# Optimization experiments

Hardware: AMD Instinct MI355X
Metric: run time of the kernel (lower is better)

Reference implementation:

```python
import jax, jax.numpy as jnp
import numpy as np

N, E, B, D = 50000, 1600000, 256, 64


def _lin(k, fan_in, fan_out):
    kw, kb = jax.random.split(k)
    bound = 1.0 / np.sqrt(fan_in)
    w = jax.random.uniform(kw, (fan_in, fan_out), jnp.float32, -bound, bound)
    b = jax.random.uniform(kb, (fan_out,), jnp.float32, -bound, bound)
    return w, b


def setup_inputs() -> dict:
    key = jax.random.key(0)
    ks = jax.random.split(key, 16)
    inp = {
        "x": jax.random.normal(ks[0], (N, D), jnp.float32),
        "edge_attr": jax.random.normal(ks[1], (E, D), jnp.float32),
        "u": jax.random.normal(ks[2], (B, D), jnp.float32),
        "edge_index": jax.random.randint(ks[3], (2, E), 0, N, jnp.int32),
        "batch": jnp.sort(jax.random.randint(ks[4], (N,), 0, B, jnp.int32)),
    }
    # three MLPs: edge (in 4D), node (in 3D), global (in 3D); dims [2D, 2D, D]
    specs = [("e", 4 * D), ("n", 3 * D), ("g", 3 * D)]
    ki = 5
    for name, in_dim in specs:
        dims = [in_dim, 2 * D, 2 * D, D]
        for li in range(3):
            w, b = _lin(ks[ki], dims[li], dims[li + 1]); ki += 1
            inp[f"{name}w{li+1}"] = w
            inp[f"{name}b{li+1}"] = b
    return inp


def _mlp(h, w1, b1, w2, b2, w3, b3):
    h = h @ w1 + b1
    h = jax.nn.relu(h) @ w2 + b2
    h = jax.nn.relu(h) @ w3 + b3
    return h


def _scatter_mean(src, idx, num_segments):
    s = jax.ops.segment_sum(src, idx, num_segments=num_segments)
    c = jax.ops.segment_sum(jnp.ones_like(src[:, :1]), idx, num_segments=num_segments)
    return s / jnp.maximum(c, 1.0)


def reference(x, edge_attr, u,
              ew1, eb1, ew2, eb2, ew3, eb3,
              nw1, nb1, nw2, nb2, nw3, nb3,
              gw1, gb1, gw2, gb2, gw3, gb3,
              edge_index, batch):
    row, col = edge_index[0], edge_index[1]
    # edge model: cat[src, dest, edge_attr, u[batch[row]]] -> MLP
    e_in = jnp.concatenate([x[row], x[col], edge_attr, u[batch[row]]], axis=1)  # [E, 4D]
    e = _mlp(e_in, ew1, eb1, ew2, eb2, ew3, eb3)  # [E, D]
    # node model: scatter_mean(edge_attr', row) cat x cat u[batch] -> MLP
    n_agg = _scatter_mean(e, row, x.shape[0])  # [N, D]
    n_in = jnp.concatenate([n_agg, x, u[batch]], axis=1)  # [N, 3D]
    xn = _mlp(n_in, nw1, nb1, nw2, nb2, nw3, nb3)  # [N, D]
    # global model: cat[u, scatter_mean(x', batch), scatter_mean(e', batch[row])]
    edge_mean = _scatter_mean(e, batch[row], u.shape[0])  # [B, D]
    node_mean = _scatter_mean(xn, batch, u.shape[0])  # [B, D]
    g_in = jnp.concatenate([u, node_mean, edge_mean], axis=1)  # [B, 3D]
    un = _mlp(g_in, gw1, gb1, gw2, gb2, gw3, gb3)  # [B, D]
    return xn, e, un
```

## Files before the change

kernel.cpp:

```cpp
#include <hip/hip_runtime.h>

#define NN 50000
#define EE 1600000
#define BBATCH 256
#define DD 64

typedef _Float16 f16;
typedef _Float16 f16x4 __attribute__((ext_vector_type(4)));
typedef _Float16 f16x8 __attribute__((ext_vector_type(8)));
typedef float f32x4 __attribute__((ext_vector_type(4)));

#define MFMA16(a,b,c) __builtin_amdgcn_mfma_f32_16x16x32_f16((a),(b),(c),0,0,0)

constexpr int EW1_RL  = 264;
constexpr int EW1_OFF = 0;
constexpr int EW2_OFF = EW1_OFF + 128 * EW1_RL;
constexpr int EW3_OFF = EW2_OFF + 128 * 136;
constexpr int EH_OFF  = EW3_OFF + 64 * 136;
constexpr int EB_OFF  = EH_OFF + 8 * 16 * 136;
constexpr int ELDS    = EB_OFF + 640;

constexpr int NW1_RL  = 200;
constexpr int NW1_OFF = 0;
constexpr int NW2_OFF = NW1_OFF + 128 * NW1_RL;
constexpr int NW3_OFF = NW2_OFF + 128 * 136;
constexpr int NH_OFF  = NW3_OFF + 64 * 136;
constexpr int NB_OFF  = NH_OFF + 4 * 32 * 136;
constexpr int NLDS    = NB_OFF + 640;

__device__ __forceinline__ f16x8 pack8(const float* __restrict__ p) {
  f32x4 a = *(const f32x4*)p;
  f32x4 b = *(const f32x4*)(p + 4);
  f16x8 r;
  r[0]=(f16)a[0]; r[1]=(f16)a[1]; r[2]=(f16)a[2]; r[3]=(f16)a[3];
  r[4]=(f16)b[0]; r[5]=(f16)b[1]; r[6]=(f16)b[2]; r[7]=(f16)b[3];
  return r;
}
__device__ __forceinline__ f16x8 pack8s(const float* __restrict__ p, float sc) {
  f32x4 a = *(const f32x4*)p;
  f32x4 b = *(const f32x4*)(p + 4);
  a = a * sc; b = b * sc;
  f16x8 r;
  r[0]=(f16)a[0]; r[1]=(f16)a[1]; r[2]=(f16)a[2]; r[3]=(f16)a[3];
  r[4]=(f16)b[0]; r[5]=(f16)b[1]; r[6]=(f16)b[2]; r[7]=(f16)b[3];
  return r;
}
__device__ __forceinline__ f16x8 cvt8(f32x4 a, f32x4 b) {
  f16x8 r;
  r[0]=(f16)a[0]; r[1]=(f16)a[1]; r[2]=(f16)a[2]; r[3]=(f16)a[3];
  r[4]=(f16)b[0]; r[5]=(f16)b[1]; r[6]=(f16)b[2]; r[7]=(f16)b[3];
  return r;
}

template<int KSL, int W1RL, int W1O, int W2O, int W3O>
__device__ __forceinline__ void mlp3_core(f16* __restrict__ sm,
    const float* __restrict__ b1l, const float* __restrict__ b2l,
    const float* __restrict__ b3l,
    const f16x8 (&A1)[2][KSL], const int hb, const int r15, const int g,
    f32x4 (&acc3)[2][4])
{
  #pragma unroll
  for (int hh = 0; hh < 2; ++hh) {
    f32x4 acc[2][4];
    #pragma unroll
    for (int nt = 0; nt < 4; ++nt) {
      const float bv = b1l[(hh*4 + nt)*16 + r15];
      acc[0][nt] = (f32x4){bv, bv, bv, bv};
      acc[1][nt] = acc[0][nt];
    }
    #pragma unroll
    for (int s = 0; s < KSL; ++s) {
      #pragma unroll
      for (int nt = 0; nt < 4; ++nt) {
        const f16x8 bf = *(const f16x8*)&sm[W1O + ((hh*4+nt)*16 + r15) * W1RL + s*32 + g*8];
        acc[0][nt] = MFMA16(A1[0][s], bf, acc[0][nt]);
        acc[1][nt] = MFMA16(A1[1][s], bf, acc[1][nt]);
      }
    }
    #pragma unroll
    for (int mt = 0; mt < 2; ++mt)
      #pragma unroll
      for (int nt = 0; nt < 4; ++nt)
        #pragma unroll
        for (int i = 0; i < 4; ++i)
          sm[hb + (mt*16 + g*4 + i)*136 + (hh*4+nt)*16 + r15] =
              (f16)fmaxf(acc[mt][nt][i], 0.f);
  }

  f16x8 A2[2][4];
  #pragma unroll
  for (int mt = 0; mt < 2; ++mt)
    #pragma unroll
    for (int s = 0; s < 4; ++s)
      A2[mt][s] = *(const f16x8*)&sm[hb + (mt*16 + r15)*136 + s*32 + g*8];

  #pragma unroll
  for (int hh = 0; hh < 2; ++hh) {
    f32x4 acc[2][4];
    #pragma unroll
    for (int nt = 0; nt < 4; ++nt) {
      const float bv = b2l[(hh*4 + nt)*16 + r15];
      acc[0][nt] = (f32x4){bv, bv, bv, bv};
      acc[1][nt] = acc[0][nt];
    }
    #pragma unroll
    for (int s = 0; s < 4; ++s) {
      #pragma unroll
      for (int nt = 0; nt < 4; ++nt) {
        const f16x8 bf = *(const f16x8*)&sm[W2O + ((hh*4+nt)*16 + r15)*136 + s*32 + g*8];
        acc[0][nt] = MFMA16(A2[0][s], bf, acc[0][nt]);
        acc[1][nt] = MFMA16(A2[1][s], bf, acc[1][nt]);
      }
    }
    #pragma unroll
    for (int mt = 0; mt < 2; ++mt)
      #pragma unroll
      for (int nt = 0; nt < 4; ++nt)
        #pragma unroll
        for (int i = 0; i < 4; ++i)
          sm[hb + (mt*16 + g*4 + i)*136 + (hh*4+nt)*16 + r15] =
              (f16)fmaxf(acc[mt][nt][i], 0.f);
  }

  f16x8 A3[2][4];
  #pragma unroll
  for (int mt = 0; mt < 2; ++mt)
    #pragma unroll
    for (int s = 0; s < 4; ++s)
      A3[mt][s] = *(const f16x8*)&sm[hb + (mt*16 + r15)*136 + s*32 + g*8];

  #pragma unroll
  for (int nt = 0; nt < 4; ++nt) {
    const float bv = b3l[nt*16 + r15];
    acc3[0][nt] = (f32x4){bv, bv, bv, bv};
    acc3[1][nt] = acc3[0][nt];
  }
  #pragma unroll
  for (int s = 0; s < 4; ++s) {
    #pragma unroll
    for (int nt = 0; nt < 4; ++nt) {
      const f16x8 bf = *(const f16x8*)&sm[W3O + (nt*16 + r15)*136 + s*32 + g*8];
      acc3[0][nt] = MFMA16(A3[0][s], bf, acc3[0][nt]);
      acc3[1][nt] = MFMA16(A3[1][s], bf, acc3[1][nt]);
    }
  }
}

__global__ void transpose_all(
    const float* __restrict__ e1, const float* __restrict__ e2, const float* __restrict__ e3,
    const float* __restrict__ n1, const float* __restrict__ n2, const float* __restrict__ n3,
    const float* __restrict__ q1, const float* __restrict__ q2, const float* __restrict__ q3,
    f16* __restrict__ dst) {
  int tid = blockIdx.x * 256 + threadIdx.x;
  const int o1=32768,o2=49152,o3=57344,o4=81920,o5=98304,o6=106496,o7=131072,o8=147456,o9=155648;
  if (tid >= o9) return;
  const float* src; int in, od, rel;
  if      (tid < o1) { src=e1; in=256; od=128; rel=tid;    }
  else if (tid < o2) { src=e2; in=128; od=128; rel=tid-o1; }
  else if (tid < o3) { src=e3; in=128; od=64;  rel=tid-o2; }
  else if (tid < o4) { src=n1; in=192; od=128; rel=tid-o3; }
  else if (tid < o5) { src=n2; in=128; od=128; rel=tid-o4; }
  else if (tid < o6) { src=n3; in=128; od=64;  rel=tid-o5; }
  else if (tid < o7) { src=q1; in=192; od=128; rel=tid-o6; }
  else if (tid < o8) { src=q2; in=128; od=128; rel=tid-o7; }
  else               { src=q3; in=128; od=64;  rel=tid-o8; }
  int o = rel / in, i = rel - o * in;
  dst[tid] = (f16)src[(size_t)i * od + o];
}

__global__ void cvt_xu(const float* __restrict__ x, const float* __restrict__ u,
                       f16* __restrict__ xh, f16* __restrict__ uh) {
  const int XT = NN * 64 / 4;
  const int UT = BBATCH * 64 / 4;
  int tid = blockIdx.x * 256 + threadIdx.x;
  for (int i = tid; i < XT; i += gridDim.x * 256) {
    f32x4 v = *(const f32x4*)&x[(size_t)i * 4];
    f16x4 h; h[0]=(f16)v[0]; h[1]=(f16)v[1]; h[2]=(f16)v[2]; h[3]=(f16)v[3];
    *(f16x4*)&xh[(size_t)i * 4] = h;
  }
  if (tid < UT) {
    f32x4 v = *(const f32x4*)&u[(size_t)tid * 4];
    f16x4 h; h[0]=(f16)v[0]; h[1]=(f16)v[1]; h[2]=(f16)v[2]; h[3]=(f16)v[3];
    *(f16x4*)&uh[(size_t)tid * 4] = h;
  }
}

__global__ void count_kernel(const int* __restrict__ ei, int* __restrict__ deg) {
  int tid = blockIdx.x * 256 + threadIdx.x;
  if (tid < EE) atomicAdd(&deg[ei[tid]], 1);
}

__global__ __launch_bounds__(1024) void scan_kernel(const int* __restrict__ deg,
                                                    int* __restrict__ offs,
                                                    int* __restrict__ cursor) {
  const int t = threadIdx.x;
  const int per = (NN + 1023) / 1024;
  const int s0 = t * per;
  int s1 = s0 + per; if (s1 > NN) s1 = NN;
  int sum = 0;
  for (int i = s0; i < s1; ++i) sum += deg[i];
  const int lane = t & 63, wid = t >> 6;
  int v = sum;
  #pragma unroll
  for (int off = 1; off < 64; off <<= 1) {
    int o = __shfl_up(v, off);
    if (lane >= off) v += o;
  }
  __shared__ int wsums[16];
  __shared__ int wexcl[16];
  if (lane == 63) wsums[wid] = v;
  __syncthreads();
  if (t == 0) { int run = 0; for (int k = 0; k < 16; ++k) { wexcl[k] = run; run += wsums[k]; } }
  __syncthreads();
  int run = wexcl[wid] + v - sum;
  for (int i = s0; i < s1; ++i) { int d = deg[i]; offs[i] = run; cursor[i] = run; run += d; }
  if (t == 1023) offs[NN] = run;
}

__global__ void fill_kernel(const int* __restrict__ ei, int* __restrict__ cursor,
                            int* __restrict__ elist) {
  int tid = blockIdx.x * 256 + threadIdx.x;
  if (tid < EE) {
    int r = ei[tid];
    int pos = atomicAdd(&cursor[r], 1);
    elist[pos] = tid;
  }
}

__global__ __launch_bounds__(512, 2) void edge_mlp_kernel(
    const f16* __restrict__ xh, const float* __restrict__ ea,
    const f16* __restrict__ uh, const int* __restrict__ ei,
    const int* __restrict__ batch,
    const f16* __restrict__ w1t, const f16* __restrict__ w2t, const f16* __restrict__ w3t,
    const float* __restrict__ b1, const float* __restrict__ b2, const float* __restrict__ b3,
    float* __restrict__ e_out)
{
  __shared__ __align__(16) f16 sm[ELDS];
  const int t = threadIdx.x;
  for (int c = t; c < 4096; c += 512) { int r = c >> 5, kc = c & 31;
    *(uint4*)&sm[EW1_OFF + r*EW1_RL + kc*8] = *(const uint4*)&w1t[r*256 + kc*8]; }
  for (int c = t; c < 2048; c += 512) { int r = c >> 4, kc = c & 15;
    *(uint4*)&sm[EW2_OFF + r*136 + kc*8] = *(const uint4*)&w2t[r*128 + kc*8]; }
  for (int c = t; c < 1024; c += 512) { int r = c >> 4, kc = c & 15;
    *(uint4*)&sm[EW3_OFF + r*136 + kc*8] = *(const uint4*)&w3t[r*128 + kc*8]; }
  float* bias = (float*)&sm[EB_OFF];
  if (t < 128) { bias[t] = b1[t]; bias[128 + t] = b2[t]; }
  else if (t < 192) { bias[256 + (t - 128)] = b3[t - 128]; }
  __syncthreads();

  const int l = t & 63, w = t >> 6;
  const int r15 = l & 15, g = l >> 4;
  const int hb = EH_OFF + w * (16 * 136);
  const int NT = EE / 256;
  const int stride = gridDim.x;
  const int t0 = blockIdx.x;

  int rC[2], cC[2], bC[2];
  int rN[2], cN[2], bN[2];
  f16x8 Bx[2][6];
  f32x4 Gea[2][2][2];

  auto issueXU = [&](const int (&rr)[2], const int (&cc)[2], const int (&bb)[2]) {
    #pragma unroll
    for (int mt = 0; mt < 2; ++mt) {
      const f16* pr = xh + (size_t)rr[mt] * 64 + g * 8;
      const f16* pc = xh + (size_t)cc[mt] * 64 + g * 8;
      const f16* pu = uh + (size_t)bb[mt] * 64 + g * 8;
      Bx[mt][0] = *(const f16x8*)pr;        Bx[mt][1] = *(const f16x8*)(pr + 32);
      Bx[mt][2] = *(const f16x8*)pc;        Bx[mt][3] = *(const f16x8*)(pc + 32);
      Bx[mt][4] = *(const f16x8*)pu;        Bx[mt][5] = *(const f16x8*)(pu + 32);
    }
  };
  auto issueEA = [&](int tt) {
    #pragma unroll
    for (int mt = 0; mt < 2; ++mt) {
      const float* pe = ea + ((size_t)(tt * 256 + w * 32 + mt * 16 + r15)) * 64 + g * 8;
      #pragma unroll
      for (int ss = 0; ss < 2; ++ss) {
        Gea[mt][ss][0] = *(const f32x4*)(pe + ss * 32);
        Gea[mt][ss][1] = *(const f32x4*)(pe + ss * 32 + 4);
      }
    }
  };

  {
    int rr[2], cc[2], bb[2];
    #pragma unroll
    for (int mt = 0; mt < 2; ++mt) {
      const int eid = t0 * 256 + w * 32 + mt * 16 + r15;
      rr[mt] = ei[eid]; cc[mt] = ei[EE + eid];
    }
    #pragma unroll
    for (int mt = 0; mt < 2; ++mt) bb[mt] = batch[rr[mt]];
    issueXU(rr, cc, bb); issueEA(t0);
    int t1 = t0 + stride; if (t1 >= NT) t1 = t0;
    #pragma unroll
    for (int mt = 0; mt < 2; ++mt) {
      const int eid = t1 * 256 + w * 32 + mt * 16 + r15;
      rC[mt] = ei[eid]; cC[mt] = ei[EE + eid];
    }
    #pragma unroll
    for (int mt = 0; mt < 2; ++mt) bC[mt] = batch[rC[mt]];
  }

  for (int tile = t0; tile < NT; tile += stride) {
    f16x8 A[2][8];
    #pragma unroll
    for (int mt = 0; mt < 2; ++mt) {
      A[mt][0] = Bx[mt][0]; A[mt][1] = Bx[mt][1];
      A[mt][2] = Bx[mt][2]; A[mt][3] = Bx[mt][3];
      A[mt][4] = cvt8(Gea[mt][0][0], Gea[mt][0][1]);
      A[mt][5] = cvt8(Gea[mt][1][0], Gea[mt][1][1]);
      A[mt][6] = Bx[mt][4]; A[mt][7] = Bx[mt][5];
    }

    int t1 = tile + stride; if (t1 >= NT) t1 = t0;
    issueXU(rC, cC, bC);
    issueEA(t1);

    int t2 = tile + 2 * stride; if (t2 >= NT) t2 = t0;
    #pragma unroll
    for (int mt = 0; mt < 2; ++mt) {
      const int eid = t2 * 256 + w * 32 + mt * 16 + r15;
      rN[mt] = ei[eid]; cN[mt] = ei[EE + eid];
    }

    f32x4 acc1[2][2][4];
    #pragma unroll
    for (int hh = 0; hh < 2; ++hh)
      #pragma unroll
      for (int nt = 0; nt < 4; ++nt) {
        const float bv = bias[hh*64 + nt*16 + r15];
        acc1[hh][0][nt] = (f32x4){bv, bv, bv, bv};
        acc1[hh][1][nt] = acc1[hh][0][nt];
      }
    #pragma unroll
    for (int s = 0; s < 8; ++s)
      #pragma unroll
      for (int hh = 0; hh < 2; ++hh)
        #pragma unroll
        for (int nt = 0; nt < 4; ++nt) {
          const f16x8 bf = *(const f16x8*)&sm[EW1_OFF + (hh*64 + nt*16 + r15)*EW1_RL + s*32 + g*8];
          acc1[hh][0][nt] = MFMA16(A[0][s], bf, acc1[hh][0][nt]);
          acc1[hh][1][nt] = MFMA16(A[1][s], bf, acc1[hh][1][nt]);
        }

    #pragma unroll
    for (int mt = 0; mt < 2; ++mt) bN[mt] = batch[rN[mt]];

    f16x8 A2[2][4];
    #pragma unroll
    for (int mt = 0; mt < 2; ++mt) {
      #pragma unroll
      for (int hh = 0; hh < 2; ++hh)
        #pragma unroll
        for (int nt = 0; nt < 4; ++nt)
          #pragma unroll
          for (int i = 0; i < 4; ++i)
            sm[hb + (g*4 + i)*136 + hh*64 + nt*16 + r15] =
                (f16)fmaxf(acc1[hh][mt][nt][i], 0.f);
      #pragma unroll
      for (int s = 0; s < 4; ++s)
        A2[mt][s] = *(const f16x8*)&sm[hb + r15*136 + s*32 + g*8];
    }

    f32x4 acc2[2][2][4];
    #pragma unroll
    for (int hh = 0; hh < 2; ++hh)
      #pragma unroll
      for (int nt = 0; nt < 4; ++nt) {
        const float bv = bias[128 + hh*64 + nt*16 + r15];
        acc2[hh][0][nt] = (f32x4){bv, bv, bv, bv};
        acc2[hh][1][nt] = acc2[hh][0][nt];
      }
    #pragma unroll
    for (int s = 0; s < 4; ++s)
      #pragma unroll
      for (int hh = 0; hh < 2; ++hh)
        #pragma unroll
        for (int nt = 0; nt < 4; ++nt) {
          const f16x8 bf = *(const f16x8*)&sm[EW2_OFF + (hh*64 + nt*16 + r15)*136 + s*32 + g*8];
          acc2[hh][0][nt] = MFMA16(A2[0][s], bf, acc2[hh][0][nt]);
          acc2[hh][1][nt] = MFMA16(A2[1][s], bf, acc2[hh][1][nt]);
        }

    f16x8 A3[2][4];
    #pragma unroll
    for (int mt = 0; mt < 2; ++mt) {
      #pragma unroll
      for (int hh = 0; hh < 2; ++hh)
        #pragma unroll
        for (int nt = 0; nt < 4; ++nt)
          #pragma unroll
          for (int i = 0; i < 4; ++i)
            sm[hb + (g*4 + i)*136 + hh*64 + nt*16 + r15] =
                (f16)fmaxf(acc2[hh][mt][nt][i], 0.f);
      #pragma unroll
      for (int s = 0; s < 4; ++s)
        A3[mt][s] = *(const f16x8*)&sm[hb + r15*136 + s*32 + g*8];
    }

    f32x4 acc3[2][4];
    #pragma unroll
    for (int nt = 0; nt < 4; ++nt) {
      const float bv = bias[256 + nt*16 + r15];
      acc3[0][nt] = (f32x4){bv, bv, bv, bv};
      acc3[1][nt] = acc3[0][nt];
    }
    #pragma unroll
    for (int s = 0; s < 4; ++s)
      #pragma unroll
      for (int nt = 0; nt < 4; ++nt) {
        const f16x8 bf = *(const f16x8*)&sm[EW3_OFF + (nt*16 + r15)*136 + s*32 + g*8];
        acc3[0][nt] = MFMA16(A3[0][s], bf, acc3[0][nt]);
        acc3[1][nt] = MFMA16(A3[1][s], bf, acc3[1][nt]);
      }

    const int base = tile * 256 + w * 32;
    #pragma unroll
    for (int mt = 0; mt < 2; ++mt)
      #pragma unroll
      for (int nt = 0; nt < 4; ++nt)
        #pragma unroll
        for (int i = 0; i < 4; ++i) {
          const int m = base + mt * 16 + g * 4 + i;
          e_out[(size_t)m * 64 + nt * 16 + r15] = acc3[mt][nt][i];
        }

    #pragma unroll
    for (int mt = 0; mt < 2; ++mt) { rC[mt] = rN[mt]; cC[mt] = cN[mt]; bC[mt] = bN[mt]; }
  }
}

__global__ void nsum_kernel(const float* __restrict__ e_src, const int* __restrict__ offs,
                            const int* __restrict__ elist, float* __restrict__ n_sum) {
  const int l = threadIdx.x & 63;
  const int wid = (blockIdx.x * blockDim.x + threadIdx.x) >> 6;
  const int nw = (gridDim.x * blockDim.x) >> 6;
  for (int node = wid; node < NN; node += nw) {
    const int s = offs[node], e = offs[node + 1];
    float acc = 0.f;
    int j = s;
    for (; j + 4 <= e; j += 4) {
      const int e0 = elist[j], e1 = elist[j+1], e2 = elist[j+2], e3 = elist[j+3];
      float v0 = e_src[(size_t)e0 * 64 + l];
      float v1 = e_src[(size_t)e1 * 64 + l];
      float v2 = e_src[(size_t)e2 * 64 + l];
      float v3 = e_src[(size_t)e3 * 64 + l];
      acc += (v0 + v1) + (v2 + v3);
    }
    for (; j < e; ++j) acc += e_src[(size_t)elist[j] * 64 + l];
    n_sum[(size_t)node * 64 + l] = acc;
  }
}

__global__ __launch_bounds__(256, 1) void node_mlp_kernel(
    const float* __restrict__ x, const float* __restrict__ u,
    const int* __restrict__ batch, const float* __restrict__ n_sum,
    const int* __restrict__ deg,
    const f16* __restrict__ w1t, const f16* __restrict__ w2t, const f16* __restrict__ w3t,
    const float* __restrict__ b1, const float* __restrict__ b2, const float* __restrict__ b3,
    float* __restrict__ xn_out)
{
  __shared__ __align__(16) f16 sm[NLDS];
  const int t = threadIdx.x;
  for (int c = t; c < 3072; c += 256) { int r = c / 24, kc = c - r * 24;
    *(uint4*)&sm[NW1_OFF + r*NW1_RL + kc*8] = *(const uint4*)&w1t[r*192 + kc*8]; }
  for (int c = t; c < 2048; c += 256) { int r = c >> 4, kc = c & 15;
    *(uint4*)&sm[NW2_OFF + r*136 + kc*8] = *(const uint4*)&w2t[r*128 + kc*8]; }
  for (int c = t; c < 1024; c += 256) { int r = c >> 4, kc = c & 15;
    *(uint4*)&sm[NW3_OFF + r*136 + kc*8] = *(const uint4*)&w3t[r*128 + kc*8]; }
  float* bias = (float*)&sm[NB_OFF];
  if (t < 128) { bias[t] = b1[t]; bias[128 + t] = b2[t]; }
  if (t < 64)  { bias[256 + t] = b3[t]; }
  __syncthreads();

  const int l = t & 63, w = t >> 6;
  const int r15 = l & 15, g = l >> 4;
  const int hb = NH_OFF + w * (32 * 136);
  const int base = blockIdx.x * 128 + w * 32;

  f16x8 A1[2][6];
  #pragma unroll
  for (int mt = 0; mt < 2; ++mt) {
    int raw = base + mt * 16 + r15;
    int node = raw < NN ? raw : NN - 1;
    float inv = 1.0f / fmaxf((float)deg[node], 1.0f);
    const float* sA = n_sum + (size_t)node * 64;
    const float* sB = x + (size_t)node * 64;
    const float* sC = u + (size_t)batch[node] * 64;
    #pragma unroll
    for (int s = 0; s < 6; ++s) {
      const int off = (s & 1) * 32 + g * 8;
      if (s < 2)      A1[mt][s] = pack8s(sA + off, inv);
      else if (s < 4) A1[mt][s] = pack8(sB + off);
      else            A1[mt][s] = pack8(sC + off);
    }
  }
  f32x4 acc3[2][4];
  mlp3_core<6, NW1_RL, NW1_OFF, NW2_OFF, NW3_OFF>(sm, bias, bias + 128, bias + 256,
                                                  A1, hb, r15, g, acc3);
  #pragma unroll
  for (int mt = 0; mt < 2; ++mt)
    #pragma unroll
    for (int nt = 0; nt < 4; ++nt)
      #pragma unroll
      for (int i = 0; i < 4; ++i) {
        const int m = base + mt * 16 + g * 4 + i;
        if (m < NN) xn_out[(size_t)m * 64 + nt * 16 + r15] = acc3[mt][nt][i];
      }
}

__global__ void bstart_kernel(const int* __restrict__ batch, int* __restrict__ bstart) {
  int tid = blockIdx.x * 256 + threadIdx.x;
  if (tid >= NN) return;
  int b = batch[tid];
  if (tid == 0) { for (int k = 0; k <= b; ++k) bstart[k] = 0; }
  else { int pb = batch[tid - 1]; for (int k = pb + 1; k <= b; ++k) bstart[k] = tid; }
  if (tid == NN - 1) { for (int k = b + 1; k <= BBATCH; ++k) bstart[k] = NN; }
}

__global__ void batch_sum_kernel(const float* __restrict__ xn, const float* __restrict__ n_sum,
                                 const int* __restrict__ deg, const int* __restrict__ bstart,
                                 float* __restrict__ nbsum, float* __restrict__ ebsum,
                                 int* __restrict__ ncnt, int* __restrict__ ecnt) {
  __shared__ float red0[256];
  __shared__ float red1[256];
  __shared__ int   redi[256];
  const int b = blockIdx.x;
  const int s = bstart[b], e = bstart[b + 1];
  const int t = threadIdx.x, c = t & 63, j0 = t >> 6;
  float xs = 0.f, ns = 0.f; int dc = 0;
  for (int j = s + j0; j < e; j += 4) {
    xs += xn[(size_t)j * 64 + c];
    ns += n_sum[(size_t)j * 64 + c];
    if (c == 0) dc += deg[j];
  }
  red0[t] = xs; red1[t] = ns; redi[t] = dc;
  __syncthreads();
  if (t < 128) { red0[t] += red0[t + 128]; red1[t] += red1[t + 128]; redi[t] += redi[t + 128]; }
  __syncthreads();
  if (t < 64) {
    float a0 = red0[t] + red0[t + 64];
    float a1 = red1[t] + red1[t + 64];
    nbsum[b * 64 + t] = a0;
    ebsum[b * 64 + t] = a1;
    if (t == 0) { ncnt[b] = e - s; ecnt[b] = redi[0] + redi[64]; }
  }
}

__global__ __launch_bounds__(256, 1) void global_mlp_kernel(
    const float* __restrict__ u, const float* __restrict__ nbsum,
    const float* __restrict__ ebsum, const int* __restrict__ ncnt,
    const int* __restrict__ ecnt,
    const f16* __restrict__ w1t, const f16* __restrict__ w2t, const f16* __restrict__ w3t,
    const float* __restrict__ b1, const float* __restrict__ b2, const float* __restrict__ b3,
    float* __restrict__ un_out)
{
  __shared__ __align__(16) f16 sm[NLDS];
  const int t = threadIdx.x;
  for (int c = t; c < 3072; c += 256) { int r = c / 24, kc = c - r * 24;
    *(uint4*)&sm[NW1_OFF + r*NW1_RL + kc*8] = *(const uint4*)&w1t[r*192 + kc*8]; }
  for (int c = t; c < 2048; c += 256) { int r = c >> 4, kc = c & 15;
    *(uint4*)&sm[NW2_OFF + r*136 + kc*8] = *(const uint4*)&w2t[r*128 + kc*8]; }
  for (int c = t; c < 1024; c += 256) { int r = c >> 4, kc = c & 15;
    *(uint4*)&sm[NW3_OFF + r*136 + kc*8] = *(const uint4*)&w3t[r*128 + kc*8]; }
  float* bias = (float*)&sm[NB_OFF];
  if (t < 128) { bias[t] = b1[t]; bias[128 + t] = b2[t]; }
  if (t < 64)  { bias[256 + t] = b3[t]; }
  __syncthreads();

  const int l = t & 63, w = t >> 6;
  const int r15 = l & 15, g = l >> 4;
  const int hb = NH_OFF + w * (32 * 136);
  const int base = blockIdx.x * 128 + w * 32;

  f16x8 A1[2][6];
  #pragma unroll
  for (int mt = 0; mt < 2; ++mt) {
    const int r = base + mt * 16 + r15;
    const float invn = 1.0f / fmaxf((float)ncnt[r], 1.0f);
    const float inve = 1.0f / fmaxf((float)ecnt[r], 1.0f);
    const float* sA = u + (size_t)r * 64;
    const float* sB = nbsum + (size_t)r * 64;
    const float* sC = ebsum + (size_t)r * 64;
    #pragma unroll
    for (int s = 0; s < 6; ++s) {
      const int off = (s & 1) * 32 + g * 8;
      if (s < 2)      A1[mt][s] = pack8(sA + off);
      else if (s < 4) A1[mt][s] = pack8s(sB + off, invn);
      else            A1[mt][s] = pack8s(sC + off, inve);
    }
  }
  f32x4 acc3[2][4];
  mlp3_core<6, NW1_RL, NW1_OFF, NW2_OFF, NW3_OFF>(sm, bias, bias + 128, bias + 256,
                                                  A1, hb, r15, g, acc3);
  #pragma unroll
  for (int mt = 0; mt < 2; ++mt)
    #pragma unroll
    for (int nt = 0; nt < 4; ++nt)
      #pragma unroll
      for (int i = 0; i < 4; ++i) {
        const int m = base + mt * 16 + g * 4 + i;
        un_out[(size_t)m * 64 + nt * 16 + r15] = acc3[mt][nt][i];
      }
}

extern "C" void kernel_launch(void* const* d_in, const int* in_sizes, int n_in,
                              void* d_out, int out_size, void* d_ws, size_t ws_size,
                              hipStream_t stream)
{
  (void)in_sizes; (void)n_in; (void)out_size; (void)ws_size;
  const float* x     = (const float*)d_in[0];
  const float* ea    = (const float*)d_in[1];
  const float* u     = (const float*)d_in[2];
  const int*   ei    = (const int*)d_in[3];
  const int*   batch = (const int*)d_in[4];
  const float* ew1 = (const float*)d_in[5];  const float* eb1 = (const float*)d_in[6];
  const float* ew2 = (const float*)d_in[7];  const float* eb2 = (const float*)d_in[8];
  const float* ew3 = (const float*)d_in[9];  const float* eb3 = (const float*)d_in[10];
  const float* nw1 = (const float*)d_in[11]; const float* nb1 = (const float*)d_in[12];
  const float* nw2 = (const float*)d_in[13]; const float* nb2 = (const float*)d_in[14];
  const float* nw3 = (const float*)d_in[15]; const float* nb3 = (const float*)d_in[16];
  const float* gw1 = (const float*)d_in[17]; const float* gb1 = (const float*)d_in[18];
  const float* gw2 = (const float*)d_in[19]; const float* gb2 = (const float*)d_in[20];
  const float* gw3 = (const float*)d_in[21]; const float* gb3 = (const float*)d_in[22];

  float* xn_out = (float*)d_out;
  float* e_out  = xn_out + (size_t)NN * DD;
  float* un_out = e_out + (size_t)EE * DD;

  char* p = (char*)d_ws;
  auto alloc = [&](size_t bytes) -> void* {
    void* r = (void*)p; p += (bytes + 255) & ~(size_t)255; return r;
  };
  f16* wtE1 = (f16*)alloc(256 * 128 * 2);
  f16* wtE2 = (f16*)alloc(128 * 128 * 2);
  f16* wtE3 = (f16*)alloc(128 * 64 * 2);
  f16* wtN1 = (f16*)alloc(192 * 128 * 2);
  f16* wtN2 = (f16*)alloc(128 * 128 * 2);
  f16* wtN3 = (f16*)alloc(128 * 64 * 2);
  f16* wtG1 = (f16*)alloc(192 * 128 * 2);
  f16* wtG2 = (f16*)alloc(128 * 128 * 2);
  f16* wtG3 = (f16*)alloc(128 * 64 * 2);
  int* deg    = (int*)alloc((size_t)NN * 4);
  int* offs   = (int*)alloc((size_t)(NN + 1) * 4);
  int* cursor = (int*)alloc((size_t)NN * 4);
  int* elist  = (int*)alloc((size_t)EE * 4);
  int* bstart = (int*)alloc((size_t)(BBATCH + 1) * 4);
  float* nbsum = (float*)alloc((size_t)BBATCH * 64 * 4);
  float* ebsum = (float*)alloc((size_t)BBATCH * 64 * 4);
  int* ncnt = (int*)alloc((size_t)BBATCH * 4);
  int* ecnt = (int*)alloc((size_t)BBATCH * 4);
  float* n_sum = (float*)alloc((size_t)NN * 64 * 4);
  f16* xh = (f16*)alloc((size_t)NN * 64 * 2);
  f16* uh = (f16*)alloc((size_t)BBATCH * 64 * 2);

  transpose_all<<<dim3(608), dim3(256), 0, stream>>>(
      ew1, ew2, ew3, nw1, nw2, nw3, gw1, gw2, gw3, wtE1);
  cvt_xu<<<dim3(1024), dim3(256), 0, stream>>>(x, u, xh, uh);

  hipMemsetAsync(deg, 0, (size_t)NN * 4, stream);
  count_kernel<<<dim3(6250), dim3(256), 0, stream>>>(ei, deg);
  scan_kernel<<<dim3(1), dim3(1024), 0, stream>>>(deg, offs, cursor);
  fill_kernel<<<dim3(6250), dim3(256), 0, stream>>>(ei, cursor, elist);

  edge_mlp_kernel<<<dim3(256), dim3(512), 0, stream>>>(
      xh, ea, uh, ei, batch, wtE1, wtE2, wtE3, eb1, eb2, eb3, e_out);

  nsum_kernel<<<dim3(2048), dim3(256), 0, stream>>>(e_out, offs, elist, n_sum);

  node_mlp_kernel<<<dim3((NN + 127) / 128), dim3(256), 0, stream>>>(
      x, u, batch, n_sum, deg, wtN1, wtN2, wtN3, nb1, nb2, nb3, xn_out);

  bstart_kernel<<<dim3((NN + 255) / 256), dim3(256), 0, stream>>>(batch, bstart);
  batch_sum_kernel<<<dim3(BBATCH), dim3(256), 0, stream>>>(
      xn_out, n_sum, deg, bstart, nbsum, ebsum, ncnt, ecnt);

  global_mlp_kernel<<<dim3(2), dim3(256), 0, stream>>>(
      u, nbsum, ebsum, ncnt, ecnt, wtG1, wtG2, wtG3, gb1, gb2, gb3, un_out);
}
```

Baseline: 785.6 us.

## Transpose edge MLP MFMA operands, widen edge blocks, persist node MLP grid

The edge MLP now swaps the MFMA operands so weights act as A and activations as B. Each lane therefore holds four consecutive output features, which allows vectorized f16x4 hidden-state writes and f32x4 stores of e_out. The hidden scratch shrinks to a 72-half stride and the block grows from 8 to 10 waves (320 edges per tile) with launch bounds aiming for 3 blocks per CU. Separately, the node-sum gather is unrolled to 8 loads in flight, and the node MLP becomes a grid-stride loop over 128 blocks. The risks are register pressure at the higher occupancy target and fewer blocks covering the node MLP.

```diff
diff --git a/kernel.cpp b/kernel.cpp
--- a/kernel.cpp
+++ b/kernel.cpp
@@ -17,7 +17,7 @@
 constexpr int EW2_OFF = EW1_OFF + 128 * EW1_RL;
 constexpr int EW3_OFF = EW2_OFF + 128 * 136;
 constexpr int EH_OFF  = EW3_OFF + 64 * 136;
-constexpr int EB_OFF  = EH_OFF + 8 * 16 * 136;
+constexpr int EB_OFF  = EH_OFF + 10 * 16 * 72;
 constexpr int ELDS    = EB_OFF + 640;
 
 constexpr int NW1_RL  = 200;
@@ -227,7 +227,7 @@
   }
 }
 
-__global__ __launch_bounds__(512, 2) void edge_mlp_kernel(
+__global__ __launch_bounds__(640, 3) void edge_mlp_kernel(
     const f16* __restrict__ xh, const float* __restrict__ ea,
     const f16* __restrict__ uh, const int* __restrict__ ei,
     const int* __restrict__ batch,
@@ -237,11 +237,11 @@
 {
   __shared__ __align__(16) f16 sm[ELDS];
   const int t = threadIdx.x;
-  for (int c = t; c < 4096; c += 512) { int r = c >> 5, kc = c & 31;
+  for (int c = t; c < 4096; c += 640) { int r = c >> 5, kc = c & 31;
     *(uint4*)&sm[EW1_OFF + r*EW1_RL + kc*8] = *(const uint4*)&w1t[r*256 + kc*8]; }
-  for (int c = t; c < 2048; c += 512) { int r = c >> 4, kc = c & 15;
+  for (int c = t; c < 2048; c += 640) { int r = c >> 4, kc = c & 15;
     *(uint4*)&sm[EW2_OFF + r*136 + kc*8] = *(const uint4*)&w2t[r*128 + kc*8]; }
-  for (int c = t; c < 1024; c += 512) { int r = c >> 4, kc = c & 15;
+  for (int c = t; c < 1024; c += 640) { int r = c >> 4, kc = c & 15;
     *(uint4*)&sm[EW3_OFF + r*136 + kc*8] = *(const uint4*)&w3t[r*128 + kc*8]; }
   float* bias = (float*)&sm[EB_OFF];
   if (t < 128) { bias[t] = b1[t]; bias[128 + t] = b2[t]; }
@@ -250,8 +250,8 @@
 
   const int l = t & 63, w = t >> 6;
   const int r15 = l & 15, g = l >> 4;
-  const int hb = EH_OFF + w * (16 * 136);
-  const int NT = EE / 256;
+  const int hb = EH_OFF + w * (16 * 72);
+  const int NT = EE / 320;
   const int stride = gridDim.x;
   const int t0 = blockIdx.x;
 
@@ -274,7 +274,7 @@
   auto issueEA = [&](int tt) {
     #pragma unroll
     for (int mt = 0; mt < 2; ++mt) {
-      const float* pe = ea + ((size_t)(tt * 256 + w * 32 + mt * 16 + r15)) * 64 + g * 8;
+      const float* pe = ea + ((size_t)(tt * 320 + w * 32 + mt * 16 + r15)) * 64 + g * 8;
       #pragma unroll
       for (int ss = 0; ss < 2; ++ss) {
         Gea[mt][ss][0] = *(const f32x4*)(pe + ss * 32);
@@ -287,7 +287,7 @@
     int rr[2], cc[2], bb[2];
     #pragma unroll
     for (int mt = 0; mt < 2; ++mt) {
-      const int eid = t0 * 256 + w * 32 + mt * 16 + r15;
+      const int eid = t0 * 320 + w * 32 + mt * 16 + r15;
       rr[mt] = ei[eid]; cc[mt] = ei[EE + eid];
     }
     #pragma unroll
@@ -296,7 +296,7 @@
     int t1 = t0 + stride; if (t1 >= NT) t1 = t0;
     #pragma unroll
     for (int mt = 0; mt < 2; ++mt) {
-      const int eid = t1 * 256 + w * 32 + mt * 16 + r15;
+      const int eid = t1 * 320 + w * 32 + mt * 16 + r15;
       rC[mt] = ei[eid]; cC[mt] = ei[EE + eid];
     }
     #pragma unroll
@@ -314,118 +314,110 @@
       A[mt][6] = Bx[mt][4]; A[mt][7] = Bx[mt][5];
     }
 
+    int t2 = tile + 2 * stride; if (t2 >= NT) t2 = t0;
+    #pragma unroll
+    for (int mt = 0; mt < 2; ++mt) {
+      const int eid = t2 * 320 + w * 32 + mt * 16 + r15;
+      rN[mt] = ei[eid]; cN[mt] = ei[EE + eid];
+    }
+
+    f32x4 acc1[2][8];
+    #pragma unroll
+    for (int a = 0; a < 8; ++a) {
+      const f32x4 bv = *(const f32x4*)&bias[a*16 + g*4];
+      acc1[0][a] = bv; acc1[1][a] = bv;
+    }
+    #pragma unroll
+    for (int s = 0; s < 8; ++s)
+      #pragma unroll
+      for (int a = 0; a < 8; ++a) {
+        const f16x8 wf = *(const f16x8*)&sm[EW1_OFF + (a*16 + r15)*EW1_RL + s*32 + g*8];
+        acc1[0][a] = MFMA16(wf, A[0][s], acc1[0][a]);
+        acc1[1][a] = MFMA16(wf, A[1][s], acc1[1][a]);
+      }
+
+    #pragma unroll
+    for (int mt = 0; mt < 2; ++mt) bN[mt] = batch[rN[mt]];
+
+    f16x8 B2[2][4];
+    #pragma unroll
+    for (int mt = 0; mt < 2; ++mt)
+      #pragma unroll
+      for (int hh = 0; hh < 2; ++hh) {
+        #pragma unroll
+        for (int ap = 0; ap < 4; ++ap) {
+          const f32x4 v = acc1[mt][hh*4 + ap];
+          f16x4 hv;
+          hv[0]=(f16)fmaxf(v[0],0.f); hv[1]=(f16)fmaxf(v[1],0.f);
+          hv[2]=(f16)fmaxf(v[2],0.f); hv[3]=(f16)fmaxf(v[3],0.f);
+          *(f16x4*)&sm[hb + r15*72 + ap*16 + g*4] = hv;
+        }
+        #pragma unroll
+        for (int sl = 0; sl < 2; ++sl)
+          B2[mt][hh*2 + sl] = *(const f16x8*)&sm[hb + r15*72 + sl*32 + g*8];
+      }
+
     int t1 = tile + stride; if (t1 >= NT) t1 = t0;
     issueXU(rC, cC, bC);
+
+    f32x4 acc2[2][8];
+    #pragma unroll
+    for (int a = 0; a < 8; ++a) {
+      const f32x4 bv = *(const f32x4*)&bias[128 + a*16 + g*4];
+      acc2[0][a] = bv; acc2[1][a] = bv;
+    }
+    #pragma unroll
+    for (int s = 0; s < 4; ++s)
+      #pragma unroll
+      for (int a = 0; a < 8; ++a) {
+        const f16x8 wf = *(const f16x8*)&sm[EW2_OFF + (a*16 + r15)*136 + s*32 + g*8];
+        acc2[0][a] = MFMA16(wf, B2[0][s], acc2[0][a]);
+        acc2[1][a] = MFMA16(wf, B2[1][s], acc2[1][a]);
+      }
+
+    f16x8 B3[2][4];
+    #pragma unroll
+    for (int mt = 0; mt < 2; ++mt)
+      #pragma unroll
+      for (int hh = 0; hh < 2; ++hh) {
+        #pragma unroll
+        for (int ap = 0; ap < 4; ++ap) {
+          const f32x4 v = acc2[mt][hh*4 + ap];
+          f16x4 hv;
+          hv[0]=(f16)fmaxf(v[0],0.f); hv[1]=(f16)fmaxf(v[1],0.f);
+          hv[2]=(f16)fmaxf(v[2],0.f); hv[3]=(f16)fmaxf(v[3],0.f);
+          *(f16x4*)&sm[hb + r15*72 + ap*16 + g*4] = hv;
+        }
+        #pragma unroll
+        for (int sl = 0; sl < 2; ++sl)
+          B3[mt][hh*2 + sl] = *(const f16x8*)&sm[hb + r15*72 + sl*32 + g*8];
+      }
+
     issueEA(t1);
 
-    int t2 = tile + 2 * stride; if (t2 >= NT) t2 = t0;
-    #pragma unroll
-    for (int mt = 0; mt < 2; ++mt) {
-      const int eid = t2 * 256 + w * 32 + mt * 16 + r15;
-      rN[mt] = ei[eid]; cN[mt] = ei[EE + eid];
-    }
-
-    f32x4 acc1[2][2][4];
-    #pragma unroll
-    for (int hh = 0; hh < 2; ++hh)
-      #pragma unroll
-      for (int nt = 0; nt < 4; ++nt) {
-        const float bv = bias[hh*64 + nt*16 + r15];
-        acc1[hh][0][nt] = (f32x4){bv, bv, bv, bv};
-        acc1[hh][1][nt] = acc1[hh][0][nt];
-      }
-    #pragma unroll
-    for (int s = 0; s < 8; ++s)
-      #pragma unroll
-      for (int hh = 0; hh < 2; ++hh)
-        #pragma unroll
-        for (int nt = 0; nt < 4; ++nt) {
-          const f16x8 bf = *(const f16x8*)&sm[EW1_OFF + (hh*64 + nt*16 + r15)*EW1_RL + s*32 + g*8];
-          acc1[hh][0][nt] = MFMA16(A[0][s], bf, acc1[hh][0][nt]);
-          acc1[hh][1][nt] = MFMA16(A[1][s], bf, acc1[hh][1][nt]);
-        }
-
-    #pragma unroll
-    for (int mt = 0; mt < 2; ++mt) bN[mt] = batch[rN[mt]];
-
-    f16x8 A2[2][4];
-    #pragma unroll
-    for (int mt = 0; mt < 2; ++mt) {
-      #pragma unroll
-      for (int hh = 0; hh < 2; ++hh)
-        #pragma unroll
-        for (int nt = 0; nt < 4; ++nt)
-          #pragma unroll
-          for (int i = 0; i < 4; ++i)
-            sm[hb + (g*4 + i)*136 + hh*64 + nt*16 + r15] =
-                (f16)fmaxf(acc1[hh][mt][nt][i], 0.f);
-      #pragma unroll
-      for (int s = 0; s < 4; ++s)
-        A2[mt][s] = *(const f16x8*)&sm[hb + r15*136 + s*32 + g*8];
-    }
-
-    f32x4 acc2[2][2][4];
-    #pragma unroll
-    for (int hh = 0; hh < 2; ++hh)
-      #pragma unroll
-      for (int nt = 0; nt < 4; ++nt) {
-        const float bv = bias[128 + hh*64 + nt*16 + r15];
-        acc2[hh][0][nt] = (f32x4){bv, bv, bv, bv};
-        acc2[hh][1][nt] = acc2[hh][0][nt];
-      }
+    f32x4 acc3[2][4];
+    #pragma unroll
+    for (int a = 0; a < 4; ++a) {
+      const f32x4 bv = *(const f32x4*)&bias[256 + a*16 + g*4];
+      acc3[0][a] = bv; acc3[1][a] = bv;
+    }
     #pragma unroll
     for (int s = 0; s < 4; ++s)
       #pragma unroll
-      for (int hh = 0; hh < 2; ++hh)
-        #pragma unroll
-        for (int nt = 0; nt < 4; ++nt) {
-          const f16x8 bf = *(const f16x8*)&sm[EW2_OFF + (hh*64 + nt*16 + r15)*136 + s*32 + g*8];
-          acc2[hh][0][nt] = MFMA16(A2[0][s], bf, acc2[hh][0][nt]);
-          acc2[hh][1][nt] = MFMA16(A2[1][s], bf, acc2[hh][1][nt]);
-        }
-
-    f16x8 A3[2][4];
-    #pragma unroll
-    for (int mt = 0; mt < 2; ++mt) {
-      #pragma unroll
-      for (int hh = 0; hh < 2; ++hh)
-        #pragma unroll
-        for (int nt = 0; nt < 4; ++nt)
-          #pragma unroll
-          for (int i = 0; i < 4; ++i)
-            sm[hb + (g*4 + i)*136 + hh*64 + nt*16 + r15] =
-                (f16)fmaxf(acc2[hh][mt][nt][i], 0.f);
-      #pragma unroll
-      for (int s = 0; s < 4; ++s)
-        A3[mt][s] = *(const f16x8*)&sm[hb + r15*136 + s*32 + g*8];
-    }
-
-    f32x4 acc3[2][4];
-    #pragma unroll
-    for (int nt = 0; nt < 4; ++nt) {
-      const float bv = bias[256 + nt*16 + r15];
-      acc3[0][nt] = (f32x4){bv, bv, bv, bv};
-      acc3[1][nt] = acc3[0][nt];
-    }
-    #pragma unroll
-    for (int s = 0; s < 4; ++s)
-      #pragma unroll
-      for (int nt = 0; nt < 4; ++nt) {
-        const f16x8 bf = *(const f16x8*)&sm[EW3_OFF + (nt*16 + r15)*136 + s*32 + g*8];
-        acc3[0][nt] = MFMA16(A3[0][s], bf, acc3[0][nt]);
-        acc3[1][nt] = MFMA16(A3[1][s], bf, acc3[1][nt]);
-      }
-
-    const int base = tile * 256 + w * 32;
-    #pragma unroll
-    for (int mt = 0; mt < 2; ++mt)
-      #pragma unroll
-      for (int nt = 0; nt < 4; ++nt)
-        #pragma unroll
-        for (int i = 0; i < 4; ++i) {
-          const int m = base + mt * 16 + g * 4 + i;
-          e_out[(size_t)m * 64 + nt * 16 + r15] = acc3[mt][nt][i];
-        }
+      for (int a = 0; a < 4; ++a) {
+        const f16x8 wf = *(const f16x8*)&sm[EW3_OFF + (a*16 + r15)*136 + s*32 + g*8];
+        acc3[0][a] = MFMA16(wf, B3[0][s], acc3[0][a]);
+        acc3[1][a] = MFMA16(wf, B3[1][s], acc3[1][a]);
+      }
+
+    const int base = tile * 320 + w * 32;
+    #pragma unroll
+    for (int mt = 0; mt < 2; ++mt) {
+      const int m = base + mt * 16 + r15;
+      #pragma unroll
+      for (int a = 0; a < 4; ++a)
+        *(f32x4*)&e_out[(size_t)m * 64 + a*16 + g*4] = acc3[mt][a];
+    }
 
     #pragma unroll
     for (int mt = 0; mt < 2; ++mt) { rC[mt] = rN[mt]; cC[mt] = cN[mt]; bC[mt] = bN[mt]; }
@@ -441,13 +433,16 @@
     const int s = offs[node], e = offs[node + 1];
     float acc = 0.f;
     int j = s;
-    for (; j + 4 <= e; j += 4) {
-      const int e0 = elist[j], e1 = elist[j+1], e2 = elist[j+2], e3 = elist[j+3];
-      float v0 = e_src[(size_t)e0 * 64 + l];
-      float v1 = e_src[(size_t)e1 * 64 + l];
-      float v2 = e_src[(size_t)e2 * 64 + l];
-      float v3 = e_src[(size_t)e3 * 64 + l];
-      acc += (v0 + v1) + (v2 + v3);
+    for (; j + 8 <= e; j += 8) {
+      float v0 = e_src[(size_t)elist[j]   * 64 + l];
+      float v1 = e_src[(size_t)elist[j+1] * 64 + l];
+      float v2 = e_src[(size_t)elist[j+2] * 64 + l];
+      float v3 = e_src[(size_t)elist[j+3] * 64 + l];
+      float v4 = e_src[(size_t)elist[j+4] * 64 + l];
+      float v5 = e_src[(size_t)elist[j+5] * 64 + l];
+      float v6 = e_src[(size_t)elist[j+6] * 64 + l];
+      float v7 = e_src[(size_t)elist[j+7] * 64 + l];
+      acc += ((v0 + v1) + (v2 + v3)) + ((v4 + v5) + (v6 + v7));
     }
     for (; j < e; ++j) acc += e_src[(size_t)elist[j] * 64 + l];
     n_sum[(size_t)node * 64 + l] = acc;
@@ -478,37 +473,40 @@
   const int l = t & 63, w = t >> 6;
   const int r15 = l & 15, g = l >> 4;
   const int hb = NH_OFF + w * (32 * 136);
-  const int base = blockIdx.x * 128 + w * 32;
-
-  f16x8 A1[2][6];
-  #pragma unroll
-  for (int mt = 0; mt < 2; ++mt) {
-    int raw = base + mt * 16 + r15;
-    int node = raw < NN ? raw : NN - 1;
-    float inv = 1.0f / fmaxf((float)deg[node], 1.0f);
-    const float* sA = n_sum + (size_t)node * 64;
-    const float* sB = x + (size_t)node * 64;
-    const float* sC = u + (size_t)batch[node] * 64;
-    #pragma unroll
-    for (int s = 0; s < 6; ++s) {
-      const int off = (s & 1) * 32 + g * 8;
-      if (s < 2)      A1[mt][s] = pack8s(sA + off, inv);
-      else if (s < 4) A1[mt][s] = pack8(sB + off);
-      else            A1[mt][s] = pack8(sC + off);
-    }
-  }
-  f32x4 acc3[2][4];
-  mlp3_core<6, NW1_RL, NW1_OFF, NW2_OFF, NW3_OFF>(sm, bias, bias + 128, bias + 256,
-                                                  A1, hb, r15, g, acc3);
-  #pragma unroll
-  for (int mt = 0; mt < 2; ++mt)
-    #pragma unroll
-    for (int nt = 0; nt < 4; ++nt)
-      #pragma unroll
-      for (int i = 0; i < 4; ++i) {
-        const int m = base + mt * 16 + g * 4 + i;
-        if (m < NN) xn_out[(size_t)m * 64 + nt * 16 + r15] = acc3[mt][nt][i];
-      }
+  const int NTT = (NN + 127) / 128;
+
+  for (int tile = blockIdx.x; tile < NTT; tile += gridDim.x) {
+    const int base = tile * 128 + w * 32;
+    f16x8 A1[2][6];
+    #pragma unroll
+    for (int mt = 0; mt < 2; ++mt) {
+      int raw = base + mt * 16 + r15;
+      int node = raw < NN ? raw : NN - 1;
+      float inv = 1.0f / fmaxf((float)deg[node], 1.0f);
+      const float* sA = n_sum + (size_t)node * 64;
+      const float* sB = x + (size_t)node * 64;
+      const float* sC = u + (size_t)batch[node] * 64;
+      #pragma unroll
+      for (int s = 0; s < 6; ++s) {
+        const int off = (s & 1) * 32 + g * 8;
+        if (s < 2)      A1[mt][s] = pack8s(sA + off, inv);
+        else if (s < 4) A1[mt][s] = pack8(sB + off);
+        else            A1[mt][s] = pack8(sC + off);
+      }
+    }
+    f32x4 acc3[2][4];
+    mlp3_core<6, NW1_RL, NW1_OFF, NW2_OFF, NW3_OFF>(sm, bias, bias + 128, bias + 256,
+                                                    A1, hb, r15, g, acc3);
+    #pragma unroll
+    for (int mt = 0; mt < 2; ++mt)
+      #pragma unroll
+      for (int nt = 0; nt < 4; ++nt)
+        #pragma unroll
+        for (int i = 0; i < 4; ++i) {
+          const int m = base + mt * 16 + g * 4 + i;
+          if (m < NN) xn_out[(size_t)m * 64 + nt * 16 + r15] = acc3[mt][nt][i];
+        }
+  }
 }
 
 __global__ void bstart_kernel(const int* __restrict__ batch, int* __restrict__ bstart) {
@@ -665,12 +663,12 @@
   scan_kernel<<<dim3(1), dim3(1024), 0, stream>>>(deg, offs, cursor);
   fill_kernel<<<dim3(6250), dim3(256), 0, stream>>>(ei, cursor, elist);
 
-  edge_mlp_kernel<<<dim3(256), dim3(512), 0, stream>>>(
+  edge_mlp_kernel<<<dim3(256), dim3(640), 0, stream>>>(
       xh, ea, uh, ei, batch, wtE1, wtE2, wtE3, eb1, eb2, eb3, e_out);
 
   nsum_kernel<<<dim3(2048), dim3(256), 0, stream>>>(e_out, offs, elist, n_sum);
 
-  node_mlp_kernel<<<dim3((NN + 127) / 128), dim3(256), 0, stream>>>(
+  node_mlp_kernel<<<dim3(128), dim3(256), 0, stream>>>(
       x, u, batch, n_sum, deg, wtN1, wtN2, wtN3, nb1, nb2, nb3, xn_out);
 
   bstart_kernel<<<dim3((NN + 255) / 256), dim3(256), 0, stream>>>(batch, bstart);
```

Result: slower. 1.012 ms, median of 3 (+28.8%).
